# Performance work log

Measured on AMD Instinct MI355X. Metric: run time of the kernel, lower is better.

The kernel has to match this reference:

```python
import jax, jax.numpy as jnp
import numpy as np

N = 4096
K = 64
E = N * K
LD = 2      # location_dim
ED = 8      # attention embed_dim
H = 256     # lck_structure width
BN_EPS = 1e-5


def setup_inputs() -> dict:
    key = jax.random.key(0)
    ks = jax.random.split(key, 12)
    coor = jax.random.normal(ks[0], (E, 2 * LD), dtype=jnp.float32)
    row = jnp.repeat(jnp.arange(N, dtype=jnp.int64), K)
    col = jax.random.randint(ks[1], (E,), 0, N, dtype=jnp.int64)
    sparse_idx = jnp.stack([row, col], axis=0)
    geodesic = jax.random.uniform(ks[2], (N, N), dtype=jnp.float32)
    angle_ratio = jax.random.uniform(ks[3], (N, N), dtype=jnp.float32)
    # LocalConditionalKer params: Linear(4,H), Linear(H,H), BN(H), Linear(H,1)
    W0 = jax.random.normal(ks[4], (2 * LD, H), dtype=jnp.float32) / np.sqrt(2 * LD)
    b0 = jnp.zeros((H,), jnp.float32)
    W1 = jax.random.normal(ks[5], (H, H), dtype=jnp.float32) / np.sqrt(H)
    b1 = jnp.zeros((H,), jnp.float32)
    gamma = jnp.ones((H,), jnp.float32)
    beta = jnp.zeros((H,), jnp.float32)
    W2 = jax.random.normal(ks[6], (H, 1), dtype=jnp.float32) / np.sqrt(H)
    b2 = jnp.zeros((1,), jnp.float32)
    # Attention params: query/key Linear(LD, ED)
    Wq = jax.random.normal(ks[7], (LD, ED), dtype=jnp.float32) / np.sqrt(LD)
    bq = jnp.zeros((ED,), jnp.float32)
    Wk = jax.random.normal(ks[8], (LD, ED), dtype=jnp.float32) / np.sqrt(LD)
    bk = jnp.zeros((ED,), jnp.float32)
    x = jax.random.normal(ks[9], (1,), dtype=jnp.float32)
    return dict(x=x, coor=coor, sparse_idx=sparse_idx, geodesic=geodesic,
                angle_ratio=angle_ratio, W0=W0, b0=b0, W1=W1, b1=b1,
                gamma=gamma, beta=beta, W2=W2, b2=b2,
                Wq=Wq, bq=bq, Wk=Wk, bk=bk)


def _lck(coor, W0, b0, W1, b1, gamma, beta, W2, b2):
    # loop semantics: activation applied before every layer except j==1
    h = jnp.tanh(coor) @ W0 + b0          # j=0: Linear(4,H)
    h = h @ W1 + b1                        # j=1: Linear(H,H), no pre-activation
    h = jnp.tanh(h)                        # j=2: BN(H) in training mode (batch stats)
    mu = jnp.mean(h, axis=0)
    var = jnp.var(h, axis=0)               # biased variance, as torch BN uses
    h = gamma * (h - mu) * jax.lax.rsqrt(var + BN_EPS) + beta
    h = jnp.tanh(h) @ W2 + b2              # j=3: Linear(H,1)
    return jax.nn.relu(h)                  # [E,1]


def reference(x, coor, sparse_idx, geodesic, angle_ratio,
              W0, b0, W1, b1, gamma, beta, W2, b2, Wq, bq, Wk, bk):
    row, col = sparse_idx[0], sparse_idx[1]
    # per-edge kernel value, scattered into dense NxN (duplicates summed)
    vals = _lck(coor, W0, b0, W1, b1, gamma, beta, W2, b2).reshape(-1)  # [E]
    lcker = jnp.zeros((N, N), vals.dtype).at[row, col].add(vals)
    # attention over neighbors
    sphere = coor[:, :LD] + coor[:, LD:]           # [E, 2]
    sphere = sphere.reshape(N, K, LD)               # [N, K, 2]
    center = sphere[:, :1, :]                       # [N, 1, 2]
    q = center @ Wq + bq                            # [N, 1, ED]
    k = sphere @ Wk + bk                            # [N, K, ED]
    att = jnp.abs(jnp.einsum('nqe,nke->nqk', q, k).squeeze(1))  # [N, K]
    alpha = jnp.zeros((N, N), att.dtype).at[row, col].add(att.reshape(-1))
    distance_decay = jnp.exp(-alpha * geodesic)
    return lcker * distance_decay * angle_ratio
```

## Files before the change

kernel.cpp:

```cpp
#include <hip/hip_runtime.h>

#define N_ 4096
#define K_ 64
#define E_ (N_*K_)
#define H_ 256
#define EPS_ 1e-5f
#define L2E_ 1.4426950408889634f
#define TL2E_ 2.8853900817779268f

#if __has_builtin(__builtin_amdgcn_exp2f)
#define EXP2(x) __builtin_amdgcn_exp2f(x)
#else
#define EXP2(x) __expf((x) * 0.6931471805599453f)
#endif

__device__ __forceinline__ float ftanh(float x) {
    float e = EXP2(x * TL2E_);
    return 1.0f - 2.0f * __builtin_amdgcn_rcpf(e + 1.0f);
}

__global__ __launch_bounds__(256) void prep_kernel(
    const float* __restrict__ W0, const float* __restrict__ b0,
    const float* __restrict__ W1, const float* __restrict__ b1,
    float* __restrict__ W01, float* __restrict__ b01)
{
    int c = threadIdx.x;
    int h0 = blockIdx.x * 8;
    float a0 = 0.f, a1 = 0.f, a2 = 0.f, a3 = 0.f, ab = 0.f;
    #pragma unroll
    for (int h = h0; h < h0 + 8; ++h) {
        float w = W1[h * H_ + c];
        a0 = fmaf(W0[0 * H_ + h], w, a0);
        a1 = fmaf(W0[1 * H_ + h], w, a1);
        a2 = fmaf(W0[2 * H_ + h], w, a2);
        a3 = fmaf(W0[3 * H_ + h], w, a3);
        ab = fmaf(b0[h], w, ab);
    }
    if (blockIdx.x == 0) ab += b1[c];
    atomicAdd(&W01[c], a0);
    atomicAdd(&W01[H_ + c], a1);
    atomicAdd(&W01[2 * H_ + c], a2);
    atomicAdd(&W01[3 * H_ + c], a3);
    atomicAdd(&b01[c], ab);
}

__global__ __launch_bounds__(256, 8) void stats_kernel(
    const float* __restrict__ coor, const float* __restrict__ W01,
    const float* __restrict__ b01, float* __restrict__ part)
{
    const int c = threadIdx.x;
    const float w0 = TL2E_ * W01[c],        w1 = TL2E_ * W01[H_ + c];
    const float w2 = TL2E_ * W01[2*H_ + c], w3 = TL2E_ * W01[3*H_ + c];
    const float bb = TL2E_ * b01[c];
    __shared__ float4 T[128];
    const int e0 = blockIdx.x * 128;
    if (c < 128) {
        float4 v = reinterpret_cast<const float4*>(coor)[e0 + c];
        T[c] = make_float4(ftanh(v.x), ftanh(v.y), ftanh(v.z), ftanh(v.w));
    }
    __syncthreads();
    float sr = 0.f, sr2 = 0.f;
    #pragma unroll 8
    for (int i = 0; i < 128; ++i) {
        float4 t = T[i];
        float u = fmaf(t.w, w3, fmaf(t.z, w2, fmaf(t.y, w1, fmaf(t.x, w0, bb))));
        float r = __builtin_amdgcn_rcpf(EXP2(u) + 1.0f);
        sr += r;
        sr2 = fmaf(r, r, sr2);
    }
    part[blockIdx.x * 512 + c] = sr;
    part[blockIdx.x * 512 + 256 + c] = sr2;
}

__global__ __launch_bounds__(512) void reduce_kernel(
    const float* __restrict__ part, float* __restrict__ sums)
{
    int t = threadIdx.x;
    int b0 = blockIdx.x * 64;
    float local = 0.f;
    #pragma unroll 8
    for (int b = b0; b < b0 + 64; ++b) local += part[b * 512 + t];
    atomicAdd(&sums[t], local);
}

__global__ __launch_bounds__(256) void finalize_kernel(
    const float* __restrict__ sums, const float* __restrict__ gamma,
    const float* __restrict__ beta, const float* __restrict__ W2,
    const float* __restrict__ b2,
    const float* __restrict__ W01, const float* __restrict__ b01,
    float* __restrict__ folded, float* __restrict__ swp)
{
    int c = threadIdx.x;
    const float inv = 1.0f / (float)E_;
    float p = sums[c] * inv;
    float q = sums[256 + c] * inv;
    float mu = 1.0f - 2.0f * p;
    float var = 4.0f * fmaf(-p, p, q);
    float a = gamma[c] * rsqrtf(var + EPS_);
    float bf = fmaf(-mu, a, beta[c]);
    folded[c * 8 + 0] = TL2E_ * W01[c];
    folded[c * 8 + 1] = TL2E_ * W01[H_ + c];
    folded[c * 8 + 2] = TL2E_ * W01[2 * H_ + c];
    folded[c * 8 + 3] = TL2E_ * W01[3 * H_ + c];
    folded[c * 8 + 4] = TL2E_ * b01[c];
    folded[c * 8 + 5] = -4.0f * L2E_ * a;
    folded[c * 8 + 6] = TL2E_ * (a + bf);
    folded[c * 8 + 7] = -2.0f * W2[c];
    __shared__ float red[256];
    red[c] = W2[c];
    __syncthreads();
    for (int s = 128; s > 0; s >>= 1) {
        if (c < s) red[c] += red[c + s];
        __syncthreads();
    }
    if (c == 0) swp[0] = red[0] + b2[0];
}

__global__ __launch_bounds__(256, 8) void edge_kernel(
    const float* __restrict__ coor, const int* __restrict__ idx,
    const float* __restrict__ folded, const float* __restrict__ swp,
    const float* __restrict__ Wq, const float* __restrict__ bq,
    const float* __restrict__ Wk, const float* __restrict__ bk,
    const float* __restrict__ geo, const float* __restrict__ ang,
    float* __restrict__ out)
{
    __shared__ float4 FS[2 * H_];
    __shared__ float4 TS[128];
    __shared__ float2 EXY[128];
    __shared__ float  ACC[8][128];

    const int t = threadIdx.x;
    const int row0 = blockIdx.x * 2;
    {
        const float4* F = reinterpret_cast<const float4*>(folded);
        FS[t] = F[t];
        FS[t + 256] = F[t + 256];
    }
    if (t < 128) {
        float4 ce = reinterpret_cast<const float4*>(coor)[row0 * K_ + t];
        TS[t] = make_float4(ftanh(ce.x), ftanh(ce.y), ftanh(ce.z), ftanh(ce.w));
        EXY[t] = make_float2(ce.x + ce.z, ce.y + ce.w);
    }
    {
        float4 z = make_float4(0.f, 0.f, 0.f, 0.f);
        float4* orow = reinterpret_cast<float4*>(out + (size_t)row0 * N_);
        #pragma unroll
        for (int i = 0; i < 8; ++i) orow[i * 256 + t] = z;
    }
    __syncthreads();

    const int eg = (t & 31) * 4;
    const int chunk = t >> 5;
    const float4 tq0 = TS[eg], tq1 = TS[eg + 1], tq2 = TS[eg + 2], tq3 = TS[eg + 3];
    const float4* Fp = &FS[chunk * 64];
    float a0 = 0.f, a1 = 0.f, a2 = 0.f, a3 = 0.f;
    #pragma unroll 4
    for (int i = 0; i < 32; ++i) {
        float4 f0 = Fp[2 * i];
        float4 f1 = Fp[2 * i + 1];
        #define EVAL(tq, ak) { \
            float u = fmaf(tq.w, f0.w, fmaf(tq.z, f0.z, fmaf(tq.y, f0.y, fmaf(tq.x, f0.x, f1.x)))); \
            float r = __builtin_amdgcn_rcpf(EXP2(u) + 1.0f); \
            float r2 = __builtin_amdgcn_rcpf(EXP2(fmaf(r, f1.y, f1.z)) + 1.0f); \
            ak = fmaf(r2, f1.w, ak); }
        EVAL(tq0, a0) EVAL(tq1, a1) EVAL(tq2, a2) EVAL(tq3, a3)
        #undef EVAL
    }
    *reinterpret_cast<float4*>(&ACC[chunk][eg]) = make_float4(a0, a1, a2, a3);
    __syncthreads();

    const int w = t >> 6, lane = t & 63;
    if (w < 2) {
        const int row = row0 + w;
        const int eb = w * 64 + lane;
        float val = swp[0];
        #pragma unroll
        for (int c = 0; c < 8; ++c) val += ACC[c][eb];
        val = fmaxf(val, 0.f);

        float2 exy = EXY[eb];
        float ex = exy.x, ey = exy.y;
        float sx = __shfl(ex, 0), sy = __shfl(ey, 0);
        float att = 0.f;
        #pragma unroll
        for (int j = 0; j < 8; ++j) {
            float qj = fmaf(sy, Wq[8 + j], fmaf(sx, Wq[j], bq[j]));
            float kj = fmaf(ey, Wk[8 + j], fmaf(ex, Wk[j], bk[j]));
            att = fmaf(qj, kj, att);
        }
        att = fabsf(att);

        const int col = idx[E_ + row * K_ + lane];
        float vsum = val, asum = att;
        bool leader = true;
        for (int j = 0; j < 64; ++j) {
            int   bc = __shfl(col, j);
            float bv = __shfl(val, j);
            float ba = __shfl(att, j);
            if (bc == col && j != lane) {
                if (j < lane) leader = false;
                else { vsum += bv; asum += ba; }
            }
        }
        if (leader) {
            size_t p = (size_t)row * N_ + col;
            out[p] = vsum * __expf(-asum * geo[p]) * ang[p];
        }
    }
}

extern "C" void kernel_launch(void* const* d_in, const int* in_sizes, int n_in,
                              void* d_out, int out_size, void* d_ws, size_t ws_size,
                              hipStream_t stream)
{
    const float* coor  = (const float*)d_in[1];
    const int*   idx   = (const int*)d_in[2];
    const float* geo   = (const float*)d_in[3];
    const float* ang   = (const float*)d_in[4];
    const float* W0    = (const float*)d_in[5];
    const float* b0    = (const float*)d_in[6];
    const float* W1    = (const float*)d_in[7];
    const float* b1    = (const float*)d_in[8];
    const float* gamma = (const float*)d_in[9];
    const float* beta  = (const float*)d_in[10];
    const float* W2    = (const float*)d_in[11];
    const float* b2    = (const float*)d_in[12];
    const float* Wq    = (const float*)d_in[13];
    const float* bq    = (const float*)d_in[14];
    const float* Wk    = (const float*)d_in[15];
    const float* bk    = (const float*)d_in[16];

    float* ws = (float*)d_ws;
    float* sums   = ws;
    float* W01    = ws + 512;
    float* b01    = ws + 1536;
    float* folded = ws + 1792;
    float* swp    = ws + 3840;
    float* part   = ws + 4096;

    hipMemsetAsync(ws, 0, 1792 * sizeof(float), stream);

    prep_kernel<<<32, 256, 0, stream>>>(W0, b0, W1, b1, W01, b01);
    stats_kernel<<<E_ / 128, 256, 0, stream>>>(coor, W01, b01, part);
    reduce_kernel<<<32, 512, 0, stream>>>(part, sums);
    finalize_kernel<<<1, 256, 0, stream>>>(sums, gamma, beta, W2, b2, W01, b01,
                                           folded, swp);
    edge_kernel<<<N_ / 2, 256, 0, stream>>>(coor, idx, folded, swp,
                                            Wq, bq, Wk, bk, geo, ang, (float*)d_out);
}
```

Before: 77.70 us.

## Drop memset and atomics; fuse BN stat reduction with fold into one kernel

Moves the W0·W1 fold into a single-block prep kernel that writes prescaled weights directly, so the workspace memset and the atomics are no longer needed. The W2 sum is computed in prep. The partial-sum reduce and the finalize step are merged into one kernel with 256 blocks, one per BN channel, which do a tree reduction. This cuts the launch count from five operations to four, but prep now runs serially on one block over 256 rows, and the per-channel reduce reads the partials with a 512-float stride.

After: 87.28 us. +12.3%, slower.

```diff
diff --git a/kernel.cpp b/kernel.cpp
--- a/kernel.cpp
+++ b/kernel.cpp
@@ -22,36 +22,43 @@
 __global__ __launch_bounds__(256) void prep_kernel(
     const float* __restrict__ W0, const float* __restrict__ b0,
     const float* __restrict__ W1, const float* __restrict__ b1,
-    float* __restrict__ W01, float* __restrict__ b01)
+    const float* __restrict__ W2, const float* __restrict__ b2,
+    float* __restrict__ W01g, float* __restrict__ swp)
 {
     int c = threadIdx.x;
-    int h0 = blockIdx.x * 8;
     float a0 = 0.f, a1 = 0.f, a2 = 0.f, a3 = 0.f, ab = 0.f;
-    #pragma unroll
-    for (int h = h0; h < h0 + 8; ++h) {
+    for (int h = 0; h < H_; ++h) {
         float w = W1[h * H_ + c];
-        a0 = fmaf(W0[0 * H_ + h], w, a0);
-        a1 = fmaf(W0[1 * H_ + h], w, a1);
+        a0 = fmaf(W0[h], w, a0);
+        a1 = fmaf(W0[H_ + h], w, a1);
         a2 = fmaf(W0[2 * H_ + h], w, a2);
         a3 = fmaf(W0[3 * H_ + h], w, a3);
         ab = fmaf(b0[h], w, ab);
     }
-    if (blockIdx.x == 0) ab += b1[c];
-    atomicAdd(&W01[c], a0);
-    atomicAdd(&W01[H_ + c], a1);
-    atomicAdd(&W01[2 * H_ + c], a2);
-    atomicAdd(&W01[3 * H_ + c], a3);
-    atomicAdd(&b01[c], ab);
+    W01g[c]          = TL2E_ * a0;
+    W01g[H_ + c]     = TL2E_ * a1;
+    W01g[2 * H_ + c] = TL2E_ * a2;
+    W01g[3 * H_ + c] = TL2E_ * a3;
+    W01g[4 * H_ + c] = TL2E_ * (ab + b1[c]);
+
+    __shared__ float red[256];
+    red[c] = W2[c];
+    __syncthreads();
+    for (int s = 128; s > 0; s >>= 1) {
+        if (c < s) red[c] += red[c + s];
+        __syncthreads();
+    }
+    if (c == 0) swp[0] = red[0] + b2[0];
 }
 
 __global__ __launch_bounds__(256, 8) void stats_kernel(
-    const float* __restrict__ coor, const float* __restrict__ W01,
-    const float* __restrict__ b01, float* __restrict__ part)
+    const float* __restrict__ coor, const float* __restrict__ W01g,
+    float* __restrict__ part)
 {
     const int c = threadIdx.x;
-    const float w0 = TL2E_ * W01[c],        w1 = TL2E_ * W01[H_ + c];
-    const float w2 = TL2E_ * W01[2*H_ + c], w3 = TL2E_ * W01[3*H_ + c];
-    const float bb = TL2E_ * b01[c];
+    const float w0 = W01g[c],          w1 = W01g[H_ + c];
+    const float w2 = W01g[2 * H_ + c], w3 = W01g[3 * H_ + c];
+    const float bb = W01g[4 * H_ + c];
     __shared__ float4 T[128];
     const int e0 = blockIdx.x * 128;
     if (c < 128) {
@@ -72,48 +79,47 @@
     part[blockIdx.x * 512 + 256 + c] = sr2;
 }
 
-__global__ __launch_bounds__(512) void reduce_kernel(
-    const float* __restrict__ part, float* __restrict__ sums)
-{
-    int t = threadIdx.x;
-    int b0 = blockIdx.x * 64;
-    float local = 0.f;
-    #pragma unroll 8
-    for (int b = b0; b < b0 + 64; ++b) local += part[b * 512 + t];
-    atomicAdd(&sums[t], local);
-}
-
-__global__ __launch_bounds__(256) void finalize_kernel(
-    const float* __restrict__ sums, const float* __restrict__ gamma,
-    const float* __restrict__ beta, const float* __restrict__ W2,
-    const float* __restrict__ b2,
-    const float* __restrict__ W01, const float* __restrict__ b01,
-    float* __restrict__ folded, float* __restrict__ swp)
-{
-    int c = threadIdx.x;
-    const float inv = 1.0f / (float)E_;
-    float p = sums[c] * inv;
-    float q = sums[256 + c] * inv;
-    float mu = 1.0f - 2.0f * p;
-    float var = 4.0f * fmaf(-p, p, q);
-    float a = gamma[c] * rsqrtf(var + EPS_);
-    float bf = fmaf(-mu, a, beta[c]);
-    folded[c * 8 + 0] = TL2E_ * W01[c];
-    folded[c * 8 + 1] = TL2E_ * W01[H_ + c];
-    folded[c * 8 + 2] = TL2E_ * W01[2 * H_ + c];
-    folded[c * 8 + 3] = TL2E_ * W01[3 * H_ + c];
-    folded[c * 8 + 4] = TL2E_ * b01[c];
-    folded[c * 8 + 5] = -4.0f * L2E_ * a;
-    folded[c * 8 + 6] = TL2E_ * (a + bf);
-    folded[c * 8 + 7] = -2.0f * W2[c];
-    __shared__ float red[256];
-    red[c] = W2[c];
+__global__ __launch_bounds__(256) void reduce_fold_kernel(
+    const float* __restrict__ part, const float* __restrict__ W01g,
+    const float* __restrict__ gamma, const float* __restrict__ beta,
+    const float* __restrict__ W2, float* __restrict__ folded)
+{
+    const int t = threadIdx.x;
+    const int j = blockIdx.x;
+    float s1 = 0.f, s2 = 0.f;
+    #pragma unroll
+    for (int k = 0; k < 8; ++k) {
+        int b = t + 256 * k;
+        s1 += part[(size_t)b * 512 + j];
+        s2 += part[(size_t)b * 512 + 256 + j];
+    }
+    __shared__ float2 RED[256];
+    RED[t] = make_float2(s1, s2);
     __syncthreads();
     for (int s = 128; s > 0; s >>= 1) {
-        if (c < s) red[c] += red[c + s];
+        if (t < s) {
+            RED[t].x += RED[t + s].x;
+            RED[t].y += RED[t + s].y;
+        }
         __syncthreads();
     }
-    if (c == 0) swp[0] = red[0] + b2[0];
+    if (t == 0) {
+        const float inv = 1.0f / (float)E_;
+        float sp = RED[0].x * inv;
+        float sq = RED[0].y * inv;
+        float mu = 1.0f - 2.0f * sp;
+        float var = 4.0f * fmaf(-sp, sp, sq);
+        float a  = gamma[j] * rsqrtf(var + EPS_);
+        float bf = fmaf(-mu, a, beta[j]);
+        folded[8 * j + 0] = W01g[j];
+        folded[8 * j + 1] = W01g[H_ + j];
+        folded[8 * j + 2] = W01g[2 * H_ + j];
+        folded[8 * j + 3] = W01g[3 * H_ + j];
+        folded[8 * j + 4] = W01g[4 * H_ + j];
+        folded[8 * j + 5] = -4.0f * L2E_ * a;
+        folded[8 * j + 6] = TL2E_ * (a + bf);
+        folded[8 * j + 7] = -2.0f * W2[j];
+    }
 }
 
 __global__ __launch_bounds__(256, 8) void edge_kernel(
@@ -230,21 +236,15 @@
     const float* Wk    = (const float*)d_in[15];
     const float* bk    = (const float*)d_in[16];
 
-    float* ws = (float*)d_ws;
-    float* sums   = ws;
-    float* W01    = ws + 512;
-    float* b01    = ws + 1536;
-    float* folded = ws + 1792;
-    float* swp    = ws + 3840;
-    float* part   = ws + 4096;
-
-    hipMemsetAsync(ws, 0, 1792 * sizeof(float), stream);
-
-    prep_kernel<<<32, 256, 0, stream>>>(W0, b0, W1, b1, W01, b01);
-    stats_kernel<<<E_ / 128, 256, 0, stream>>>(coor, W01, b01, part);
-    reduce_kernel<<<32, 512, 0, stream>>>(part, sums);
-    finalize_kernel<<<1, 256, 0, stream>>>(sums, gamma, beta, W2, b2, W01, b01,
-                                           folded, swp);
+    float* ws     = (float*)d_ws;
+    float* swp    = ws;
+    float* W01g   = ws + 256;
+    float* folded = ws + 2048;
+    float* part   = ws + 8192;
+
+    prep_kernel<<<1, 256, 0, stream>>>(W0, b0, W1, b1, W2, b2, W01g, swp);
+    stats_kernel<<<E_ / 128, 256, 0, stream>>>(coor, W01g, part);
+    reduce_fold_kernel<<<256, 256, 0, stream>>>(part, W01g, gamma, beta, W2, folded);
     edge_kernel<<<N_ / 2, 256, 0, stream>>>(coor, idx, folded, swp,
                                             Wq, bq, Wk, bk, geo, ang, (float*)d_out);
 }
```

## Retile edge MLP to 8 edges per thread and speed up duplicate merge

Applied to the files above, without the earlier changes.

Each thread now evaluates 8 edges over 16 hidden units instead of 4 edges over 32. The tanh inputs move to structure-of-arrays in LDS and the folded weights are padded to avoid bank conflicts. The attention score and column indices are computed early and kept in LDS. The geo/ang loads are issued before the duplicate merge, and the 64-iteration shuffle loop becomes an LDS-based match mask plus a loop over actual duplicates only. The intent is to reuse each weight load across more edges and cut the per-edge merge cost, at the price of more registers and a 16-way reduction.

Result: no change. 76.38 us (-1.7%).

```diff
diff --git a/kernel.cpp b/kernel.cpp
--- a/kernel.cpp
+++ b/kernel.cpp
@@ -124,62 +124,29 @@
     const float* __restrict__ geo, const float* __restrict__ ang,
     float* __restrict__ out)
 {
-    __shared__ float4 FS[2 * H_];
-    __shared__ float4 TS[128];
-    __shared__ float2 EXY[128];
-    __shared__ float  ACC[8][128];
+    __shared__ float4 FS[2 * H_ + 16];
+    __shared__ float  TSx[128], TSy[128], TSz[128], TSw[128];
+    __shared__ float  ACC[16][128];
+    __shared__ int    COL[128];
+    __shared__ float  ATT[128];
 
     const int t = threadIdx.x;
     const int row0 = blockIdx.x * 2;
+    const int eb0 = blockIdx.x * 128;
+
     {
         const float4* F = reinterpret_cast<const float4*>(folded);
-        FS[t] = F[t];
-        FS[t + 256] = F[t + 256];
-    }
+        FS[t + (t >> 5)] = F[t];
+        int j = t + 256;
+        FS[j + (j >> 5)] = F[j];
+    }
+    int col = 0;
     if (t < 128) {
-        float4 ce = reinterpret_cast<const float4*>(coor)[row0 * K_ + t];
-        TS[t] = make_float4(ftanh(ce.x), ftanh(ce.y), ftanh(ce.z), ftanh(ce.w));
-        EXY[t] = make_float2(ce.x + ce.z, ce.y + ce.w);
-    }
-    {
-        float4 z = make_float4(0.f, 0.f, 0.f, 0.f);
-        float4* orow = reinterpret_cast<float4*>(out + (size_t)row0 * N_);
-        #pragma unroll
-        for (int i = 0; i < 8; ++i) orow[i * 256 + t] = z;
-    }
-    __syncthreads();
-
-    const int eg = (t & 31) * 4;
-    const int chunk = t >> 5;
-    const float4 tq0 = TS[eg], tq1 = TS[eg + 1], tq2 = TS[eg + 2], tq3 = TS[eg + 3];
-    const float4* Fp = &FS[chunk * 64];
-    float a0 = 0.f, a1 = 0.f, a2 = 0.f, a3 = 0.f;
-    #pragma unroll 4
-    for (int i = 0; i < 32; ++i) {
-        float4 f0 = Fp[2 * i];
-        float4 f1 = Fp[2 * i + 1];
-        #define EVAL(tq, ak) { \
-            float u = fmaf(tq.w, f0.w, fmaf(tq.z, f0.z, fmaf(tq.y, f0.y, fmaf(tq.x, f0.x, f1.x)))); \
-            float r = __builtin_amdgcn_rcpf(EXP2(u) + 1.0f); \
-            float r2 = __builtin_amdgcn_rcpf(EXP2(fmaf(r, f1.y, f1.z)) + 1.0f); \
-            ak = fmaf(r2, f1.w, ak); }
-        EVAL(tq0, a0) EVAL(tq1, a1) EVAL(tq2, a2) EVAL(tq3, a3)
-        #undef EVAL
-    }
-    *reinterpret_cast<float4*>(&ACC[chunk][eg]) = make_float4(a0, a1, a2, a3);
-    __syncthreads();
-
-    const int w = t >> 6, lane = t & 63;
-    if (w < 2) {
-        const int row = row0 + w;
-        const int eb = w * 64 + lane;
-        float val = swp[0];
-        #pragma unroll
-        for (int c = 0; c < 8; ++c) val += ACC[c][eb];
-        val = fmaxf(val, 0.f);
-
-        float2 exy = EXY[eb];
-        float ex = exy.x, ey = exy.y;
+        float4 ce = reinterpret_cast<const float4*>(coor)[eb0 + t];
+        TSx[t] = ftanh(ce.x); TSy[t] = ftanh(ce.y);
+        TSz[t] = ftanh(ce.z); TSw[t] = ftanh(ce.w);
+        col = idx[E_ + eb0 + t];
+        float ex = ce.x + ce.z, ey = ce.y + ce.w;
         float sx = __shfl(ex, 0), sy = __shfl(ey, 0);
         float att = 0.f;
         #pragma unroll
@@ -188,23 +155,91 @@
             float kj = fmaf(ey, Wk[8 + j], fmaf(ex, Wk[j], bk[j]));
             att = fmaf(qj, kj, att);
         }
-        att = fabsf(att);
-
-        const int col = idx[E_ + row * K_ + lane];
-        float vsum = val, asum = att;
-        bool leader = true;
-        for (int j = 0; j < 64; ++j) {
-            int   bc = __shfl(col, j);
+        COL[t] = col;
+        ATT[t] = fabsf(att);
+    }
+    {
+        float4 z = make_float4(0.f, 0.f, 0.f, 0.f);
+        float4* orow = reinterpret_cast<float4*>(out + (size_t)row0 * N_);
+        #pragma unroll
+        for (int i = 0; i < 8; ++i) orow[i * 256 + t] = z;
+    }
+    __syncthreads();
+
+    const int eg = (t & 15) * 8;
+    const int chunk = t >> 4;
+    float4 xa = *reinterpret_cast<const float4*>(&TSx[eg]);
+    float4 xb = *reinterpret_cast<const float4*>(&TSx[eg + 4]);
+    float4 ya = *reinterpret_cast<const float4*>(&TSy[eg]);
+    float4 yb = *reinterpret_cast<const float4*>(&TSy[eg + 4]);
+    float4 za = *reinterpret_cast<const float4*>(&TSz[eg]);
+    float4 zb = *reinterpret_cast<const float4*>(&TSz[eg + 4]);
+    float4 wa = *reinterpret_cast<const float4*>(&TSw[eg]);
+    float4 wb = *reinterpret_cast<const float4*>(&TSw[eg + 4]);
+    const float4* Fp = &FS[chunk * 33];
+    float ac0 = 0.f, ac1 = 0.f, ac2 = 0.f, ac3 = 0.f;
+    float ac4 = 0.f, ac5 = 0.f, ac6 = 0.f, ac7 = 0.f;
+    #define EVAL(tx_, ty_, tz_, tw_, ak) { \
+        float u = fmaf(tw_, f0.w, fmaf(tz_, f0.z, fmaf(ty_, f0.y, fmaf(tx_, f0.x, f1.x)))); \
+        float r = __builtin_amdgcn_rcpf(EXP2(u) + 1.0f); \
+        float r2 = __builtin_amdgcn_rcpf(EXP2(fmaf(r, f1.y, f1.z)) + 1.0f); \
+        ak = fmaf(r2, f1.w, ak); }
+    #pragma unroll 4
+    for (int i = 0; i < 16; ++i) {
+        float4 f0 = Fp[2 * i];
+        float4 f1 = Fp[2 * i + 1];
+        EVAL(xa.x, ya.x, za.x, wa.x, ac0)
+        EVAL(xa.y, ya.y, za.y, wa.y, ac1)
+        EVAL(xa.z, ya.z, za.z, wa.z, ac2)
+        EVAL(xa.w, ya.w, za.w, wa.w, ac3)
+        EVAL(xb.x, yb.x, zb.x, wb.x, ac4)
+        EVAL(xb.y, yb.y, zb.y, wb.y, ac5)
+        EVAL(xb.z, yb.z, zb.z, wb.z, ac6)
+        EVAL(xb.w, yb.w, zb.w, wb.w, ac7)
+    }
+    #undef EVAL
+    *reinterpret_cast<float4*>(&ACC[chunk][eg])     = make_float4(ac0, ac1, ac2, ac3);
+    *reinterpret_cast<float4*>(&ACC[chunk][eg + 4]) = make_float4(ac4, ac5, ac6, ac7);
+    __syncthreads();
+
+    const int w = t >> 6, lane = t & 63;
+    if (w < 2) {
+        float val = swp[0];
+        #pragma unroll
+        for (int c = 0; c < 16; ++c) val += ACC[c][t];
+        val = fmaxf(val, 0.f);
+
+        size_t p = (size_t)(row0 + w) * N_ + col;
+        float g = geo[p], an = ang[p];
+
+        const int rb = w * 64;
+        unsigned long long m = 0;
+        float asum = 0.f;
+        #pragma unroll 8
+        for (int j4 = 0; j4 < 16; ++j4) {
+            int4   c4 = *reinterpret_cast<const int4*>(&COL[rb + 4 * j4]);
+            float4 a4 = *reinterpret_cast<const float4*>(&ATT[rb + 4 * j4]);
+            m |= (unsigned long long)(c4.x == col) << (4 * j4 + 0);
+            m |= (unsigned long long)(c4.y == col) << (4 * j4 + 1);
+            m |= (unsigned long long)(c4.z == col) << (4 * j4 + 2);
+            m |= (unsigned long long)(c4.w == col) << (4 * j4 + 3);
+            asum += (c4.x == col) ? a4.x : 0.f;
+            asum += (c4.y == col) ? a4.y : 0.f;
+            asum += (c4.z == col) ? a4.z : 0.f;
+            asum += (c4.w == col) ? a4.w : 0.f;
+        }
+        bool leader = ((m & ((1ull << lane) - 1ull)) == 0ull);
+
+        float vsum = val;
+        unsigned long long m2 = m & ~(1ull << lane);
+        while (__any(m2 != 0ull)) {
+            unsigned long long pick = m2 ? m2 : 1ull;
+            int j = __ffsll(pick) - 1;
             float bv = __shfl(val, j);
-            float ba = __shfl(att, j);
-            if (bc == col && j != lane) {
-                if (j < lane) leader = false;
-                else { vsum += bv; asum += ba; }
-            }
+            if (m2) { vsum += bv; m2 &= m2 - 1; }
         }
         if (leader) {
-            size_t p = (size_t)row * N_ + col;
-            out[p] = vsum * __expf(-asum * geo[p]) * ang[p];
+            out[p] = vsum * __expf(-asum * g) * an;
         }
     }
 }
```
